# Optimization experiments

Measured on AMD Instinct MI355X. Metric: run time of the kernel, lower is better.

Reference implementation:

```python
import jax, jax.numpy as jnp
import numpy as np

N_ACTOR = 128
NUM_MODS = 6
NUM_PTS = 30
N = 32768
B = 64
EPS = 1e-5


def _gn(x, g, b):
    # torch GroupNorm(1, C) on [..., C]: normalize over channel axis, affine
    m = jnp.mean(x, axis=-1, keepdims=True)
    v = jnp.mean((x - m) ** 2, axis=-1, keepdims=True)
    return (x - m) * jax.lax.rsqrt(v + EPS) * g + b


def setup_inputs() -> dict:
    key = jax.random.key(0)
    ks = jax.random.split(key, 32)
    d = N_ACTOR
    M = NUM_MODS
    s = 0.05
    rn = lambda k, shp: jax.random.normal(k, shp, jnp.float32) * s
    inp = {
        'actors': jax.random.normal(ks[0], (N, d), jnp.float32),
        'actor_ctrs': jax.random.normal(ks[1], (N, 2), jnp.float32),
        'actor_idcs': jnp.arange(N, dtype=jnp.int32).reshape(B, N // B),
        # per-mode residual MLP + output linear (stacked over modes)
        'pred_W1': rn(ks[2], (M, d, d)),
        'pred_g1': jnp.ones((M, d), jnp.float32),
        'pred_b1': jnp.zeros((M, d), jnp.float32),
        'pred_W2': rn(ks[3], (M, d, d)),
        'pred_g2': jnp.ones((M, d), jnp.float32),
        'pred_b2': jnp.zeros((M, d), jnp.float32),
        'pred_Wo': rn(ks[4], (M, d, 2 * NUM_PTS)),
        'pred_bo': rn(ks[5], (M, 2 * NUM_PTS)),
        # cls head: residual MLP + Linear(d,1)
        'cls_W1': rn(ks[6], (d, d)),
        'cls_g1': jnp.ones((d,), jnp.float32),
        'cls_b1': jnp.zeros((d,), jnp.float32),
        'cls_W2': rn(ks[7], (d, d)),
        'cls_g2': jnp.ones((d,), jnp.float32),
        'cls_b2': jnp.zeros((d,), jnp.float32),
        'cls_Wo': rn(ks[8], (d, 1)),
        'cls_bo': rn(ks[9], (1,)),
        # AttDest
        'att_dW1': rn(ks[10], (2, d)),
        'att_db1': rn(ks[11], (d,)),
        'att_dW2': rn(ks[12], (d, d)),
        'att_dg2': jnp.ones((d,), jnp.float32),
        'att_db2': jnp.zeros((d,), jnp.float32),
        'att_aW': rn(ks[13], (2 * d, d)),
        'att_ag': jnp.ones((d,), jnp.float32),
        'att_ab': jnp.zeros((d,), jnp.float32),
    }
    return inp


def reference(actors, actor_ctrs, actor_idcs, pred_W1, pred_g1, pred_b1,
              pred_W2, pred_g2, pred_b2, pred_Wo, pred_bo,
              cls_W1, cls_g1, cls_b1, cls_W2, cls_g2, cls_b2, cls_Wo, cls_bo,
              att_dW1, att_db1, att_dW2, att_dg2, att_db2,
              att_aW, att_ag, att_ab):
    n = actors.shape[0]
    M = pred_W1.shape[0]
    h = jnp.einsum('nc,mcd->mnd', actors, pred_W1)              # [M,N,d]
    h = jax.nn.relu(_gn(h, pred_g1[:, None, :], pred_b1[:, None, :]))
    h = _gn(jnp.einsum('mnd,mde->mne', h, pred_W2),
            pred_g2[:, None, :], pred_b2[:, None, :])
    h = jax.nn.relu(h + actors[None])                           # residual
    preds = jnp.einsum('mnd,mdo->mno', h, pred_Wo) + pred_bo[:, None, :]
    reg = preds.transpose(1, 0, 2).reshape(n, M, NUM_PTS, 2)    # [N,M,T,2]
    # per-scene reg[idcs] += ctrs: actor_idcs partitions arange(N), so this
    # is exactly a per-actor broadcast add of the (concatenated) centers
    reg = reg + actor_ctrs[:, None, None, :]
    dest_ctrs = jax.lax.stop_gradient(reg[:, :, -1, :])         # .detach()
    # --- AttDest ---
    dist = (actor_ctrs[:, None, :] - dest_ctrs).reshape(-1, 2)  # [N*M,2]
    dist = jax.nn.relu(dist @ att_dW1 + att_db1)
    dist = jax.nn.relu(_gn(dist @ att_dW2, att_dg2, att_db2))
    agts = jnp.broadcast_to(actors[:, None, :], (n, M, actors.shape[1]))
    agts = agts.reshape(-1, actors.shape[1])
    feats = jax.nn.relu(_gn(jnp.concatenate([dist, agts], axis=1) @ att_aW,
                            att_ag, att_ab))                    # [N*M,d]
    # --- cls head ---
    c = jax.nn.relu(_gn(feats @ cls_W1, cls_g1, cls_b1))
    c = _gn(c @ cls_W2, cls_g2, cls_b2)
    c = jax.nn.relu(c + feats)
    cls = (c @ cls_Wo + cls_bo).reshape(n, M)
    # --- sort modes by descending score, reorder reg accordingly ---
    order = jnp.argsort(-cls, axis=1)
    cls = jnp.take_along_axis(cls, order, axis=1)
    reg = jnp.take_along_axis(reg, order[:, :, None, None], axis=1)
    # train_model=True concatenates the per-scene splits back in order,
    # which reproduces the full arrays
    return cls, reg
```

## Files before the change

kernel.cpp:

```cpp
#include <hip/hip_runtime.h>

#define EPSV 1e-5f
#define CLS_SZ (32768*6)
#define FWS_FLOATS ((size_t)196608 * 128)

#define AL(ch,row) (((ch)<<7) + ((row) ^ ((((ch)&15))<<3)))

__device__ __forceinline__ float4 ld4(const float* p) { return *reinterpret_cast<const float4*>(p); }
__device__ __forceinline__ void st4(float* p, float4 v) { *reinterpret_cast<float4*>(p) = v; }

__device__ __forceinline__ void ldW2(const float* __restrict__ Wg, int k0, int jg4,
                                     float4 (&w0)[2], float4 (&w1)[2])
{
  #pragma unroll
  for (int kk = 0; kk < 2; ++kk) {
    w0[kk] = ld4(Wg + (k0 + kk)*128 + jg4);
    w1[kk] = ld4(Wg + (k0 + kk)*128 + 64 + jg4);
  }
}

__device__ __forceinline__ void fma2(const float* X, int k0, int ag,
                                     const float4 (&w0)[2], const float4 (&w1)[2],
                                     float (&acc)[8][8])
{
  #pragma unroll
  for (int kk = 0; kk < 2; ++kk) {
    int k = k0 + kk;
    const float* xp = X + (k<<7) + ((ag<<3) ^ ((k & 15)<<3));
    float4 x0 = ld4(xp), x1 = ld4(xp + 4);
    float xv[8] = {x0.x,x0.y,x0.z,x0.w,x1.x,x1.y,x1.z,x1.w};
    float wv[8] = {w0[kk].x,w0[kk].y,w0[kk].z,w0[kk].w,
                   w1[kk].x,w1[kk].y,w1[kk].z,w1[kk].w};
    #pragma unroll
    for (int r = 0; r < 8; ++r)
      #pragma unroll
      for (int c2 = 0; c2 < 8; ++c2)
        acc[r][c2] = fmaf(xv[r], wv[c2], acc[r][c2]);
  }
}

__device__ __forceinline__ void gemmR(const float* X, const float* __restrict__ Wg,
                                      float (&acc)[8][8], int ag, int jg4)
{
  float4 a0[2], a1[2], b0[2], b1[2];
  ldW2(Wg, 0, jg4, a0, a1);
  #pragma unroll 1
  for (int c = 0; c < 64; c += 2) {
    ldW2(Wg, (c+1)*2, jg4, b0, b1);
    fma2(X, c*2, ag, a0, a1, acc);
    if (c + 2 < 64) ldW2(Wg, (c+2)*2, jg4, a0, a1);
    fma2(X, (c+1)*2, ag, b0, b1, acc);
  }
}

__device__ __forceinline__ void ldWo(const float* __restrict__ Wg, int k0, int jg,
                                     bool ldw, float4 (&w)[8])
{
  #pragma unroll
  for (int kk = 0; kk < 8; ++kk)
    w[kk] = ldw ? ld4(Wg + (k0 + kk)*60 + jg*4) : make_float4(0.f,0.f,0.f,0.f);
}

__device__ __forceinline__ void fmaWo(const float* X, int k0, int ag,
                                      const float4 (&w)[8], float (&acc)[8][4])
{
  #pragma unroll
  for (int kk = 0; kk < 8; ++kk) {
    int k = k0 + kk;
    const float* xp = X + (k<<7) + ((ag<<3) ^ ((k & 15)<<3));
    float4 x0 = ld4(xp), x1 = ld4(xp + 4);
    float xv[8] = {x0.x,x0.y,x0.z,x0.w,x1.x,x1.y,x1.z,x1.w};
    float wv[4] = {w[kk].x,w[kk].y,w[kk].z,w[kk].w};
    #pragma unroll
    for (int r = 0; r < 8; ++r)
      #pragma unroll
      for (int c2 = 0; c2 < 4; ++c2)
        acc[r][c2] = fmaf(xv[r], wv[c2], acc[r][c2]);
  }
}

__device__ __forceinline__ void gemmWoR(const float* X, const float* __restrict__ Wg,
                                        float (&acc)[8][4], int ag, int jg)
{
  const bool ldw = (jg < 15);
  float4 a[8], b[8];
  ldWo(Wg, 0, jg, ldw, a);
  #pragma unroll 1
  for (int c = 0; c < 16; c += 2) {
    ldWo(Wg, (c+1)*8, jg, ldw, b);
    fmaWo(X, c*8, ag, a, acc);
    if (c + 2 < 16) ldWo(Wg, (c+2)*8, jg, ldw, a);
    fmaWo(X, (c+1)*8, ag, b, acc);
  }
}

__device__ __forceinline__ void gn_finish(float* PS1, float* PS2, float* MEAN, float* RSTD, int tid)
{
  __syncthreads();
  if (tid < 128) {
    float a = 0.f, b = 0.f;
    #pragma unroll
    for (int j = 0; j < 4; ++j) { a += PS1[tid*4 + j]; b += PS2[tid*4 + j]; }
    float mu = a * 0.0078125f;
    float var = b * 0.0078125f - mu*mu;
    MEAN[tid] = mu;
    RSTD[tid] = rsqrtf(var + EPSV);
  }
  __syncthreads();
}

__device__ __forceinline__ void gn_reduce8(const float (&acc)[8][8], float* PS1, float* PS2,
                                           float* MEAN, float* RSTD, int ag, int jg, int tid)
{
  #pragma unroll
  for (int r = 0; r < 8; ++r) {
    float s = 0.f, q = 0.f;
    #pragma unroll
    for (int c = 0; c < 8; ++c) { float v = acc[r][c]; s += v; q += v*v; }
    s += __shfl_xor(s, 1, 64); q += __shfl_xor(q, 1, 64);
    s += __shfl_xor(s, 2, 64); q += __shfl_xor(q, 2, 64);
    if ((jg & 3) == 0) { int row = ag*8 + r; PS1[row*4 + (jg>>2)] = s; PS2[row*4 + (jg>>2)] = q; }
  }
  gn_finish(PS1, PS2, MEAN, RSTD, tid);
}

__global__ void __launch_bounds__(256, 2) pred_kernel(
    const float* __restrict__ actors, const float* __restrict__ ctrs,
    const float* __restrict__ W1, const float* __restrict__ g1v, const float* __restrict__ b1v,
    const float* __restrict__ W2, const float* __restrict__ g2v, const float* __restrict__ b2v,
    const float* __restrict__ Wo, const float* __restrict__ bov,
    float* __restrict__ out_reg)
{
  __shared__ __align__(16) float ACT[16384];
  __shared__ float PS1[512], PS2[512], MEAN[128], RSTD[128];

  const int tid = threadIdx.x;
  const int jg = tid & 15, ag = tid >> 4;
  const int jg4 = jg*4;
  const int m  = blockIdx.y;
  const int n0 = blockIdx.x * 128;

  #pragma unroll
  for (int p = 0; p < 16; ++p) {
    int i = (p<<8) + tid;
    int r = i >> 5, q4 = (i & 31) << 2;
    float4 v = ld4(actors + (size_t)(n0 + r)*128 + q4);
    ACT[AL(q4+0, r)] = v.x; ACT[AL(q4+1, r)] = v.y;
    ACT[AL(q4+2, r)] = v.z; ACT[AL(q4+3, r)] = v.w;
  }
  __syncthreads();

  float acc[8][8];
  #pragma unroll
  for (int r = 0; r < 8; ++r)
    #pragma unroll
    for (int c = 0; c < 8; ++c) acc[r][c] = 0.f;

  gemmR(ACT, W1 + (size_t)m*16384, acc, ag, jg4);
  gn_reduce8(acc, PS1, PS2, MEAN, RSTD, ag, jg, tid);
  {
    float mu[8], rs[8];
    #pragma unroll
    for (int r = 0; r < 8; ++r) { mu[r] = MEAN[ag*8+r]; rs[r] = RSTD[ag*8+r]; }
    float4 gl = ld4(g1v + m*128 + jg4), gh = ld4(g1v + m*128 + 64 + jg4);
    float4 bl = ld4(b1v + m*128 + jg4), bh = ld4(b1v + m*128 + 64 + jg4);
    float gv[8] = {gl.x,gl.y,gl.z,gl.w,gh.x,gh.y,gh.z,gh.w};
    float bv[8] = {bl.x,bl.y,bl.z,bl.w,bh.x,bh.y,bh.z,bh.w};
    float vm[8][8];
    #pragma unroll
    for (int r = 0; r < 8; ++r)
      #pragma unroll
      for (int c = 0; c < 8; ++c)
        vm[r][c] = fmaxf((acc[r][c] - mu[r]) * rs[r] * gv[c] + bv[c], 0.f);
    #pragma unroll
    for (int c = 0; c < 8; ++c) {
      int ch = (c < 4) ? (jg4 + c) : (64 + jg4 + (c - 4));
      int base = (ch<<7) + ((ag<<3) ^ ((ch & 15)<<3));
      st4(ACT + base,     make_float4(vm[0][c],vm[1][c],vm[2][c],vm[3][c]));
      st4(ACT + base + 4, make_float4(vm[4][c],vm[5][c],vm[6][c],vm[7][c]));
    }
  }
  __syncthreads();

  #pragma unroll
  for (int r = 0; r < 8; ++r)
    #pragma unroll
    for (int c = 0; c < 8; ++c) acc[r][c] = 0.f;

  gemmR(ACT, W2 + (size_t)m*16384, acc, ag, jg4);
  gn_reduce8(acc, PS1, PS2, MEAN, RSTD, ag, jg, tid);
  {
    float mu[8], rs[8];
    #pragma unroll
    for (int r = 0; r < 8; ++r) { mu[r] = MEAN[ag*8+r]; rs[r] = RSTD[ag*8+r]; }
    float4 gl = ld4(g2v + m*128 + jg4), gh = ld4(g2v + m*128 + 64 + jg4);
    float4 bl = ld4(b2v + m*128 + jg4), bh = ld4(b2v + m*128 + 64 + jg4);
    float gv[8] = {gl.x,gl.y,gl.z,gl.w,gh.x,gh.y,gh.z,gh.w};
    float bv[8] = {bl.x,bl.y,bl.z,bl.w,bh.x,bh.y,bh.z,bh.w};
    float vm[8][8];
    #pragma unroll
    for (int r = 0; r < 8; ++r) {
      const float* ap = actors + (size_t)(n0 + ag*8 + r)*128;
      float4 a0 = ld4(ap + jg4), a1 = ld4(ap + 64 + jg4);
      float av[8] = {a0.x,a0.y,a0.z,a0.w,a1.x,a1.y,a1.z,a1.w};
      #pragma unroll
      for (int c = 0; c < 8; ++c)
        vm[r][c] = fmaxf((acc[r][c] - mu[r]) * rs[r] * gv[c] + bv[c] + av[c], 0.f);
    }
    #pragma unroll
    for (int c = 0; c < 8; ++c) {
      int ch = (c < 4) ? (jg4 + c) : (64 + jg4 + (c - 4));
      int base = (ch<<7) + ((ag<<3) ^ ((ch & 15)<<3));
      st4(ACT + base,     make_float4(vm[0][c],vm[1][c],vm[2][c],vm[3][c]));
      st4(ACT + base + 4, make_float4(vm[4][c],vm[5][c],vm[6][c],vm[7][c]));
    }
  }
  __syncthreads();

  float acc2[8][4];
  #pragma unroll
  for (int r = 0; r < 8; ++r)
    #pragma unroll
    for (int c = 0; c < 4; ++c) acc2[r][c] = 0.f;
  gemmWoR(ACT, Wo + (size_t)m*7680, acc2, ag, jg);

  if (jg < 15) {
    float4 bo4 = ld4(bov + m*60 + jg4);
    #pragma unroll
    for (int r = 0; r < 8; ++r) {
      int n = n0 + ag*8 + r;
      float2 cc = *reinterpret_cast<const float2*>(ctrs + 2*n);
      float4 v;
      v.x = acc2[r][0] + bo4.x + cc.x;
      v.y = acc2[r][1] + bo4.y + cc.y;
      v.z = acc2[r][2] + bo4.z + cc.x;
      v.w = acc2[r][3] + bo4.w + cc.y;
      st4(out_reg + (size_t)n*360 + m*60 + jg4, v);
    }
  }
}

__global__ void __launch_bounds__(256, 2) att_feats_kernel(
    const float* __restrict__ actors, const float* __restrict__ ctrs,
    const float* __restrict__ dW1, const float* __restrict__ db1,
    const float* __restrict__ dW2, const float* __restrict__ dg2, const float* __restrict__ db2,
    const float* __restrict__ aW, const float* __restrict__ aG, const float* __restrict__ aB,
    const float* __restrict__ reg, float* __restrict__ fws)
{
  __shared__ __align__(16) float ACT[16384];
  __shared__ float PS1[512], PS2[512], MEAN[128], RSTD[128];
  float* D0x = MEAN;
  float* D0y = RSTD;

  const int tid = threadIdx.x;
  const int jg = tid & 15, ag = tid >> 4;
  const int jg4 = jg*4;
  const int r0 = blockIdx.x * 128;

  if (tid < 128) {
    int rg = r0 + tid;
    int n = rg / 6, mm = rg - 6*n;
    size_t base = (size_t)n*360 + mm*60;
    float2 c2 = *reinterpret_cast<const float2*>(ctrs + 2*n);
    D0x[tid] = c2.x - reg[base + 58];
    D0y[tid] = c2.y - reg[base + 59];
  }
  __syncthreads();

  {
    float dx[8], dy[8];
    #pragma unroll
    for (int r = 0; r < 8; ++r) { dx[r] = D0x[ag*8+r]; dy[r] = D0y[ag*8+r]; }
    #pragma unroll
    for (int c = 0; c < 8; ++c) {
      int ch = (c < 4) ? (jg4 + c) : (64 + jg4 + (c - 4));
      float w1 = dW1[ch], w2 = dW1[128 + ch], bb = db1[ch];
      float v[8];
      #pragma unroll
      for (int r = 0; r < 8; ++r) v[r] = fmaxf(fmaf(dx[r], w1, fmaf(dy[r], w2, bb)), 0.f);
      int base = (ch<<7) + ((ag<<3) ^ ((ch & 15)<<3));
      st4(ACT + base,     make_float4(v[0],v[1],v[2],v[3]));
      st4(ACT + base + 4, make_float4(v[4],v[5],v[6],v[7]));
    }
  }
  __syncthreads();

  float acc[8][8];
  #pragma unroll
  for (int r = 0; r < 8; ++r)
    #pragma unroll
    for (int c = 0; c < 8; ++c) acc[r][c] = 0.f;

  gemmR(ACT, dW2, acc, ag, jg4);
  gn_reduce8(acc, PS1, PS2, MEAN, RSTD, ag, jg, tid);
  {
    float mu[8], rs[8];
    #pragma unroll
    for (int r = 0; r < 8; ++r) { mu[r] = MEAN[ag*8+r]; rs[r] = RSTD[ag*8+r]; }
    float4 gl = ld4(dg2 + jg4), gh = ld4(dg2 + 64 + jg4);
    float4 bl = ld4(db2 + jg4), bh = ld4(db2 + 64 + jg4);
    float gv[8] = {gl.x,gl.y,gl.z,gl.w,gh.x,gh.y,gh.z,gh.w};
    float bv[8] = {bl.x,bl.y,bl.z,bl.w,bh.x,bh.y,bh.z,bh.w};
    float vm[8][8];
    #pragma unroll
    for (int r = 0; r < 8; ++r)
      #pragma unroll
      for (int c = 0; c < 8; ++c)
        vm[r][c] = fmaxf((acc[r][c] - mu[r]) * rs[r] * gv[c] + bv[c], 0.f);
    #pragma unroll
    for (int c = 0; c < 8; ++c) {
      int ch = (c < 4) ? (jg4 + c) : (64 + jg4 + (c - 4));
      int base = (ch<<7) + ((ag<<3) ^ ((ch & 15)<<3));
      st4(ACT + base,     make_float4(vm[0][c],vm[1][c],vm[2][c],vm[3][c]));
      st4(ACT + base + 4, make_float4(vm[4][c],vm[5][c],vm[6][c],vm[7][c]));
    }
  }
  __syncthreads();

  #pragma unroll
  for (int r = 0; r < 8; ++r)
    #pragma unroll
    for (int c = 0; c < 8; ++c) acc[r][c] = 0.f;
  gemmR(ACT, aW, acc, ag, jg4);
  __syncthreads();
  #pragma unroll
  for (int p = 0; p < 16; ++p) {
    int i = (p<<8) + tid;
    int r = i >> 5, q4 = (i & 31) << 2;
    int n = (r0 + r) / 6;
    float4 v = ld4(actors + (size_t)n*128 + q4);
    ACT[AL(q4+0, r)] = v.x; ACT[AL(q4+1, r)] = v.y;
    ACT[AL(q4+2, r)] = v.z; ACT[AL(q4+3, r)] = v.w;
  }
  __syncthreads();
  gemmR(ACT, aW + 16384, acc, ag, jg4);
  gn_reduce8(acc, PS1, PS2, MEAN, RSTD, ag, jg, tid);
  {
    float mu[8], rs[8];
    #pragma unroll
    for (int r = 0; r < 8; ++r) { mu[r] = MEAN[ag*8+r]; rs[r] = RSTD[ag*8+r]; }
    float4 gl = ld4(aG + jg4), gh = ld4(aG + 64 + jg4);
    float4 bl = ld4(aB + jg4), bh = ld4(aB + 64 + jg4);
    float gv[8] = {gl.x,gl.y,gl.z,gl.w,gh.x,gh.y,gh.z,gh.w};
    float bv[8] = {bl.x,bl.y,bl.z,bl.w,bh.x,bh.y,bh.z,bh.w};
    #pragma unroll
    for (int r = 0; r < 8; ++r) {
      float fv[8];
      #pragma unroll
      for (int c = 0; c < 8; ++c)
        fv[c] = fmaxf((acc[r][c] - mu[r]) * rs[r] * gv[c] + bv[c], 0.f);
      float* fp = fws + (size_t)(r0 + ag*8 + r)*128;
      st4(fp + jg4,      make_float4(fv[0],fv[1],fv[2],fv[3]));
      st4(fp + 64 + jg4, make_float4(fv[4],fv[5],fv[6],fv[7]));
    }
  }
}

__global__ void __launch_bounds__(256, 2) att_cls2_kernel(
    const float* __restrict__ cW1, const float* __restrict__ cg1, const float* __restrict__ cb1,
    const float* __restrict__ cW2, const float* __restrict__ cg2, const float* __restrict__ cb2,
    const float* __restrict__ cWo, const float* __restrict__ cbo,
    const float* __restrict__ fws, float* __restrict__ cls_out)
{
  __shared__ __align__(16) float ACT[16384];
  __shared__ float PS1[512], PS2[512], MEAN[128], RSTD[128];

  const int tid = threadIdx.x;
  const int jg = tid & 15, ag = tid >> 4;
  const int jg4 = jg*4;
  const int r0 = blockIdx.x * 128;

  #pragma unroll
  for (int p = 0; p < 16; ++p) {
    int i = (p<<8) + tid;
    int r = i >> 5, q4 = (i & 31) << 2;
    float4 v = ld4(fws + (size_t)(r0 + r)*128 + q4);
    ACT[AL(q4+0, r)] = v.x; ACT[AL(q4+1, r)] = v.y;
    ACT[AL(q4+2, r)] = v.z; ACT[AL(q4+3, r)] = v.w;
  }
  __syncthreads();

  float acc[8][8];
  #pragma unroll
  for (int r = 0; r < 8; ++r)
    #pragma unroll
    for (int c = 0; c < 8; ++c) acc[r][c] = 0.f;

  gemmR(ACT, cW1, acc, ag, jg4);
  gn_reduce8(acc, PS1, PS2, MEAN, RSTD, ag, jg, tid);
  {
    float mu[8], rs[8];
    #pragma unroll
    for (int r = 0; r < 8; ++r) { mu[r] = MEAN[ag*8+r]; rs[r] = RSTD[ag*8+r]; }
    float4 gl = ld4(cg1 + jg4), gh = ld4(cg1 + 64 + jg4);
    float4 bl = ld4(cb1 + jg4), bh = ld4(cb1 + 64 + jg4);
    float gv[8] = {gl.x,gl.y,gl.z,gl.w,gh.x,gh.y,gh.z,gh.w};
    float bv[8] = {bl.x,bl.y,bl.z,bl.w,bh.x,bh.y,bh.z,bh.w};
    float vm[8][8];
    #pragma unroll
    for (int r = 0; r < 8; ++r)
      #pragma unroll
      for (int c = 0; c < 8; ++c)
        vm[r][c] = fmaxf((acc[r][c] - mu[r]) * rs[r] * gv[c] + bv[c], 0.f);
    #pragma unroll
    for (int c = 0; c < 8; ++c) {
      int ch = (c < 4) ? (jg4 + c) : (64 + jg4 + (c - 4));
      int base = (ch<<7) + ((ag<<3) ^ ((ch & 15)<<3));
      st4(ACT + base,     make_float4(vm[0][c],vm[1][c],vm[2][c],vm[3][c]));
      st4(ACT + base + 4, make_float4(vm[4][c],vm[5][c],vm[6][c],vm[7][c]));
    }
  }
  __syncthreads();

  #pragma unroll
  for (int r = 0; r < 8; ++r)
    #pragma unroll
    for (int c = 0; c < 8; ++c) acc[r][c] = 0.f;
  gemmR(ACT, cW2, acc, ag, jg4);
  gn_reduce8(acc, PS1, PS2, MEAN, RSTD, ag, jg, tid);
  {
    float mu[8], rs[8];
    #pragma unroll
    for (int r = 0; r < 8; ++r) { mu[r] = MEAN[ag*8+r]; rs[r] = RSTD[ag*8+r]; }
    float4 gl = ld4(cg2 + jg4), gh = ld4(cg2 + 64 + jg4);
    float4 bl = ld4(cb2 + jg4), bh = ld4(cb2 + 64 + jg4);
    float4 wl = ld4(cWo + jg4), wh = ld4(cWo + 64 + jg4);
    float gv[8] = {gl.x,gl.y,gl.z,gl.w,gh.x,gh.y,gh.z,gh.w};
    float bv[8] = {bl.x,bl.y,bl.z,bl.w,bh.x,bh.y,bh.z,bh.w};
    float wv[8] = {wl.x,wl.y,wl.z,wl.w,wh.x,wh.y,wh.z,wh.w};
    #pragma unroll
    for (int r = 0; r < 8; ++r) {
      const float* fp = fws + (size_t)(r0 + ag*8 + r)*128;
      float4 a0 = ld4(fp + jg4), a1 = ld4(fp + 64 + jg4);
      float av[8] = {a0.x,a0.y,a0.z,a0.w,a1.x,a1.y,a1.z,a1.w};
      float p = 0.f;
      #pragma unroll
      for (int c = 0; c < 8; ++c) {
        float v = (acc[r][c] - mu[r]) * rs[r] * gv[c] + bv[c];
        v = fmaxf(v + av[c], 0.f);
        p = fmaf(v, wv[c], p);
      }
      float s = p;
      s += __shfl_xor(s, 1, 64);
      s += __shfl_xor(s, 2, 64);
      if ((jg & 3) == 0) PS1[(ag*8+r)*4 + (jg>>2)] = s;
    }
  }
  __syncthreads();
  if (tid < 128) {
    float s = 0.f;
    #pragma unroll
    for (int j = 0; j < 4; ++j) s += PS1[tid*4 + j];
    cls_out[r0 + tid] = s + cbo[0];
  }
}

__global__ void __launch_bounds__(256, 2) att_cls_mono_kernel(
    const float* __restrict__ actors, const float* __restrict__ ctrs,
    const float* __restrict__ dW1, const float* __restrict__ db1,
    const float* __restrict__ dW2, const float* __restrict__ dg2, const float* __restrict__ db2,
    const float* __restrict__ aW, const float* __restrict__ aG, const float* __restrict__ aB,
    const float* __restrict__ cW1, const float* __restrict__ cg1, const float* __restrict__ cb1,
    const float* __restrict__ cW2, const float* __restrict__ cg2, const float* __restrict__ cb2,
    const float* __restrict__ cWo, const float* __restrict__ cbo,
    const float* __restrict__ reg, float* __restrict__ cls_out)
{
  __shared__ __align__(16) float ACT[16384];
  __shared__ float PS1[512], PS2[512], MEAN[128], RSTD[128];
  float* D0x = MEAN;
  float* D0y = RSTD;

  const int tid = threadIdx.x;
  const int jg = tid & 15, ag = tid >> 4;
  const int jg4 = jg*4;
  const int r0 = blockIdx.x * 128;

  if (tid < 128) {
    int rg = r0 + tid;
    int n = rg / 6, mm = rg - 6*n;
    size_t base = (size_t)n*360 + mm*60;
    float2 c2 = *reinterpret_cast<const float2*>(ctrs + 2*n);
    D0x[tid] = c2.x - reg[base + 58];
    D0y[tid] = c2.y - reg[base + 59];
  }
  __syncthreads();

  {
    float dx[8], dy[8];
    #pragma unroll
    for (int r = 0; r < 8; ++r) { dx[r] = D0x[ag*8+r]; dy[r] = D0y[ag*8+r]; }
    #pragma unroll
    for (int c = 0; c < 8; ++c) {
      int ch = (c < 4) ? (jg4 + c) : (64 + jg4 + (c - 4));
      float w1 = dW1[ch], w2 = dW1[128 + ch], bb = db1[ch];
      float v[8];
      #pragma unroll
      for (int r = 0; r < 8; ++r) v[r] = fmaxf(fmaf(dx[r], w1, fmaf(dy[r], w2, bb)), 0.f);
      int base = (ch<<7) + ((ag<<3) ^ ((ch & 15)<<3));
      st4(ACT + base,     make_float4(v[0],v[1],v[2],v[3]));
      st4(ACT + base + 4, make_float4(v[4],v[5],v[6],v[7]));
    }
  }
  __syncthreads();

  float acc[8][8];
  #pragma unroll
  for (int r = 0; r < 8; ++r)
    #pragma unroll
    for (int c = 0; c < 8; ++c) acc[r][c] = 0.f;

  gemmR(ACT, dW2, acc, ag, jg4);
  gn_reduce8(acc, PS1, PS2, MEAN, RSTD, ag, jg, tid);
  {
    float mu[8], rs[8];
    #pragma unroll
    for (int r = 0; r < 8; ++r) { mu[r] = MEAN[ag*8+r]; rs[r] = RSTD[ag*8+r]; }
    float4 gl = ld4(dg2 + jg4), gh = ld4(dg2 + 64 + jg4);
    float4 bl = ld4(db2 + jg4), bh = ld4(db2 + 64 + jg4);
    float gv[8] = {gl.x,gl.y,gl.z,gl.w,gh.x,gh.y,gh.z,gh.w};
    float bv[8] = {bl.x,bl.y,bl.z,bl.w,bh.x,bh.y,bh.z,bh.w};
    float vm[8][8];
    #pragma unroll
    for (int r = 0; r < 8; ++r)
      #pragma unroll
      for (int c = 0; c < 8; ++c)
        vm[r][c] = fmaxf((acc[r][c] - mu[r]) * rs[r] * gv[c] + bv[c], 0.f);
    #pragma unroll
    for (int c = 0; c < 8; ++c) {
      int ch = (c < 4) ? (jg4 + c) : (64 + jg4 + (c - 4));
      int base = (ch<<7) + ((ag<<3) ^ ((ch & 15)<<3));
      st4(ACT + base,     make_float4(vm[0][c],vm[1][c],vm[2][c],vm[3][c]));
      st4(ACT + base + 4, make_float4(vm[4][c],vm[5][c],vm[6][c],vm[7][c]));
    }
  }
  __syncthreads();

  #pragma unroll
  for (int r = 0; r < 8; ++r)
    #pragma unroll
    for (int c = 0; c < 8; ++c) acc[r][c] = 0.f;
  gemmR(ACT, aW, acc, ag, jg4);
  __syncthreads();
  #pragma unroll
  for (int p = 0; p < 16; ++p) {
    int i = (p<<8) + tid;
    int r = i >> 5, q4 = (i & 31) << 2;
    int n = (r0 + r) / 6;
    float4 v = ld4(actors + (size_t)n*128 + q4);
    ACT[AL(q4+0, r)] = v.x; ACT[AL(q4+1, r)] = v.y;
    ACT[AL(q4+2, r)] = v.z; ACT[AL(q4+3, r)] = v.w;
  }
  __syncthreads();
  gemmR(ACT, aW + 16384, acc, ag, jg4);
  gn_reduce8(acc, PS1, PS2, MEAN, RSTD, ag, jg, tid);
  float feats[8][8];
  {
    float mu[8], rs[8];
    #pragma unroll
    for (int r = 0; r < 8; ++r) { mu[r] = MEAN[ag*8+r]; rs[r] = RSTD[ag*8+r]; }
    float4 gl = ld4(aG + jg4), gh = ld4(aG + 64 + jg4);
    float4 bl = ld4(aB + jg4), bh = ld4(aB + 64 + jg4);
    float gv[8] = {gl.x,gl.y,gl.z,gl.w,gh.x,gh.y,gh.z,gh.w};
    float bv[8] = {bl.x,bl.y,bl.z,bl.w,bh.x,bh.y,bh.z,bh.w};
    #pragma unroll
    for (int r = 0; r < 8; ++r)
      #pragma unroll
      for (int c = 0; c < 8; ++c)
        feats[r][c] = fmaxf((acc[r][c] - mu[r]) * rs[r] * gv[c] + bv[c], 0.f);
    #pragma unroll
    for (int c = 0; c < 8; ++c) {
      int ch = (c < 4) ? (jg4 + c) : (64 + jg4 + (c - 4));
      int base = (ch<<7) + ((ag<<3) ^ ((ch & 15)<<3));
      st4(ACT + base,     make_float4(feats[0][c],feats[1][c],feats[2][c],feats[3][c]));
      st4(ACT + base + 4, make_float4(feats[4][c],feats[5][c],feats[6][c],feats[7][c]));
    }
  }
  __syncthreads();

  #pragma unroll
  for (int r = 0; r < 8; ++r)
    #pragma unroll
    for (int c = 0; c < 8; ++c) acc[r][c] = 0.f;
  gemmR(ACT, cW1, acc, ag, jg4);
  gn_reduce8(acc, PS1, PS2, MEAN, RSTD, ag, jg, tid);
  {
    float mu[8], rs[8];
    #pragma unroll
    for (int r = 0; r < 8; ++r) { mu[r] = MEAN[ag*8+r]; rs[r] = RSTD[ag*8+r]; }
    float4 gl = ld4(cg1 + jg4), gh = ld4(cg1 + 64 + jg4);
    float4 bl = ld4(cb1 + jg4), bh = ld4(cb1 + 64 + jg4);
    float gv[8] = {gl.x,gl.y,gl.z,gl.w,gh.x,gh.y,gh.z,gh.w};
    float bv[8] = {bl.x,bl.y,bl.z,bl.w,bh.x,bh.y,bh.z,bh.w};
    float vm[8][8];
    #pragma unroll
    for (int r = 0; r < 8; ++r)
      #pragma unroll
      for (int c = 0; c < 8; ++c)
        vm[r][c] = fmaxf((acc[r][c] - mu[r]) * rs[r] * gv[c] + bv[c], 0.f);
    #pragma unroll
    for (int c = 0; c < 8; ++c) {
      int ch = (c < 4) ? (jg4 + c) : (64 + jg4 + (c - 4));
      int base = (ch<<7) + ((ag<<3) ^ ((ch & 15)<<3));
      st4(ACT + base,     make_float4(vm[0][c],vm[1][c],vm[2][c],vm[3][c]));
      st4(ACT + base + 4, make_float4(vm[4][c],vm[5][c],vm[6][c],vm[7][c]));
    }
  }
  __syncthreads();

  #pragma unroll
  for (int r = 0; r < 8; ++r)
    #pragma unroll
    for (int c = 0; c < 8; ++c) acc[r][c] = 0.f;
  gemmR(ACT, cW2, acc, ag, jg4);
  gn_reduce8(acc, PS1, PS2, MEAN, RSTD, ag, jg, tid);
  {
    float mu[8], rs[8], p[8];
    #pragma unroll
    for (int r = 0; r < 8; ++r) { mu[r] = MEAN[ag*8+r]; rs[r] = RSTD[ag*8+r]; p[r] = 0.f; }
    float4 gl = ld4(cg2 + jg4), gh = ld4(cg2 + 64 + jg4);
    float4 bl = ld4(cb2 + jg4), bh = ld4(cb2 + 64 + jg4);
    float4 wl = ld4(cWo + jg4), wh = ld4(cWo + 64 + jg4);
    float gv[8] = {gl.x,gl.y,gl.z,gl.w,gh.x,gh.y,gh.z,gh.w};
    float bv[8] = {bl.x,bl.y,bl.z,bl.w,bh.x,bh.y,bh.z,bh.w};
    float wv[8] = {wl.x,wl.y,wl.z,wl.w,wh.x,wh.y,wh.z,wh.w};
    #pragma unroll
    for (int c = 0; c < 8; ++c) {
      #pragma unroll
      for (int r = 0; r < 8; ++r) {
        float v = (acc[r][c] - mu[r]) * rs[r] * gv[c] + bv[c];
        v = fmaxf(v + feats[r][c], 0.f);
        p[r] = fmaf(v, wv[c], p[r]);
      }
    }
    #pragma unroll
    for (int r = 0; r < 8; ++r) {
      float s = p[r];
      s += __shfl_xor(s, 1, 64);
      s += __shfl_xor(s, 2, 64);
      if ((jg & 3) == 0) PS1[(ag*8+r)*4 + (jg>>2)] = s;
    }
  }
  __syncthreads();
  if (tid < 128) {
    float s = 0.f;
    #pragma unroll
    for (int j = 0; j < 4; ++j) s += PS1[tid*4 + j];
    cls_out[r0 + tid] = s + cbo[0];
  }
}

__global__ void __launch_bounds__(256) sort_kernel(float* __restrict__ out)
{
  __shared__ float RL[64*360];
  __shared__ float CL[64*6];
  __shared__ float CS[64*6];
  __shared__ int   ORD[64*6];

  const int tid = threadIdx.x;
  const int n0 = blockIdx.x * 64;
  float* regp = out + CLS_SZ;

  for (int i = tid; i < 64*360; i += 256) RL[i] = regp[(size_t)n0*360 + i];
  for (int i = tid; i < 384; i += 256)    CL[i] = out[n0*6 + i];
  __syncthreads();

  if (tid < 64) {
    float v[6];
    #pragma unroll
    for (int m2 = 0; m2 < 6; ++m2) v[m2] = CL[tid*6 + m2];
    int used = 0;
    for (int j = 0; j < 6; ++j) {
      int best = -1; float bv = 0.f;
      for (int m2 = 0; m2 < 6; ++m2) {
        if (used & (1 << m2)) continue;
        if (best < 0 || v[m2] > bv) { best = m2; bv = v[m2]; }
      }
      used |= (1 << best);
      ORD[tid*6 + j] = best;
      CS[tid*6 + j] = bv;
    }
  }
  __syncthreads();

  for (int i = tid; i < 384; i += 256) out[n0*6 + i] = CS[i];
  for (int i = tid; i < 64*360; i += 256) {
    int rl = i / 360, rem = i - rl*360;
    int slot = rem / 60, j = rem - slot*60;
    out[CLS_SZ + (size_t)n0*360 + i] = RL[rl*360 + ORD[rl*6 + slot]*60 + j];
  }
}

extern "C" void kernel_launch(void* const* d_in, const int* in_sizes, int n_in,
                              void* d_out, int out_size, void* d_ws, size_t ws_size,
                              hipStream_t stream)
{
  (void)in_sizes; (void)n_in; (void)out_size;
  const float* actors = (const float*)d_in[0];
  const float* ctrs   = (const float*)d_in[1];
  const float* pW1 = (const float*)d_in[3];
  const float* pg1 = (const float*)d_in[4];
  const float* pb1 = (const float*)d_in[5];
  const float* pW2 = (const float*)d_in[6];
  const float* pg2 = (const float*)d_in[7];
  const float* pb2 = (const float*)d_in[8];
  const float* pWo = (const float*)d_in[9];
  const float* pbo = (const float*)d_in[10];
  const float* cW1 = (const float*)d_in[11];
  const float* cg1 = (const float*)d_in[12];
  const float* cb1 = (const float*)d_in[13];
  const float* cW2 = (const float*)d_in[14];
  const float* cg2 = (const float*)d_in[15];
  const float* cb2 = (const float*)d_in[16];
  const float* cWo = (const float*)d_in[17];
  const float* cbo = (const float*)d_in[18];
  const float* dW1 = (const float*)d_in[19];
  const float* db1 = (const float*)d_in[20];
  const float* dW2 = (const float*)d_in[21];
  const float* dg2 = (const float*)d_in[22];
  const float* db2 = (const float*)d_in[23];
  const float* aW  = (const float*)d_in[24];
  const float* aG  = (const float*)d_in[25];
  const float* aB  = (const float*)d_in[26];

  float* out = (float*)d_out;
  float* out_reg = out + CLS_SZ;
  float* fws = (float*)d_ws;
  const bool split = ws_size >= FWS_FLOATS * sizeof(float);

  dim3 gA(256, 6);
  pred_kernel<<<gA, 256, 0, stream>>>(actors, ctrs, pW1, pg1, pb1, pW2, pg2, pb2,
                                      pWo, pbo, out_reg);
  if (split) {
    att_feats_kernel<<<1536, 256, 0, stream>>>(actors, ctrs,
                                               dW1, db1, dW2, dg2, db2,
                                               aW, aG, aB, out_reg, fws);
    att_cls2_kernel<<<1536, 256, 0, stream>>>(cW1, cg1, cb1, cW2, cg2, cb2,
                                              cWo, cbo, fws, out);
  } else {
    att_cls_mono_kernel<<<1536, 256, 0, stream>>>(actors, ctrs,
                                                  dW1, db1, dW2, dg2, db2,
                                                  aW, aG, aB,
                                                  cW1, cg1, cb1, cW2, cg2, cb2, cWo, cbo,
                                                  out_reg, out);
  }
  sort_kernel<<<512, 256, 0, stream>>>(out);
}
```

Measured before the change: 789.9 us.

## Shrink row tile to 64 rows per block to raise occupancy

New measurement: 934.6 us. 18.3% more time.

```diff
diff --git a/kernel.cpp b/kernel.cpp
--- a/kernel.cpp
+++ b/kernel.cpp
@@ -5,6 +5,7 @@
 #define FWS_FLOATS ((size_t)196608 * 128)
 
 #define AL(ch,row) (((ch)<<7) + ((row) ^ ((((ch)&15))<<3)))
+#define AL64(ch,row) (((ch)<<6) + ((row) ^ ((((ch)&7))<<3)))
 
 __device__ __forceinline__ float4 ld4(const float* p) { return *reinterpret_cast<const float4*>(p); }
 __device__ __forceinline__ void st4(float* p, float4 v) { *reinterpret_cast<float4*>(p) = v; }
@@ -16,6 +17,432 @@
   for (int kk = 0; kk < 2; ++kk) {
     w0[kk] = ld4(Wg + (k0 + kk)*128 + jg4);
     w1[kk] = ld4(Wg + (k0 + kk)*128 + 64 + jg4);
+  }
+}
+
+__device__ __forceinline__ void fma2_64(const float* X, int k0, int ag,
+                                        const float4 (&w0)[2], const float4 (&w1)[2],
+                                        float (&acc)[4][8])
+{
+  #pragma unroll
+  for (int kk = 0; kk < 2; ++kk) {
+    int k = k0 + kk;
+    float4 x = ld4(X + (k<<6) + ((ag<<2) ^ ((k & 7)<<3)));
+    float xv[4] = {x.x,x.y,x.z,x.w};
+    float wv[8] = {w0[kk].x,w0[kk].y,w0[kk].z,w0[kk].w,
+                   w1[kk].x,w1[kk].y,w1[kk].z,w1[kk].w};
+    #pragma unroll
+    for (int r = 0; r < 4; ++r)
+      #pragma unroll
+      for (int c2 = 0; c2 < 8; ++c2)
+        acc[r][c2] = fmaf(xv[r], wv[c2], acc[r][c2]);
+  }
+}
+
+__device__ __forceinline__ void gemmR64(const float* X, const float* __restrict__ Wg,
+                                        float (&acc)[4][8], int ag, int jg4)
+{
+  float4 a0[2], a1[2], b0[2], b1[2];
+  ldW2(Wg, 0, jg4, a0, a1);
+  #pragma unroll 1
+  for (int c = 0; c < 64; c += 2) {
+    ldW2(Wg, (c+1)*2, jg4, b0, b1);
+    fma2_64(X, c*2, ag, a0, a1, acc);
+    if (c + 2 < 64) ldW2(Wg, (c+2)*2, jg4, a0, a1);
+    fma2_64(X, (c+1)*2, ag, b0, b1, acc);
+  }
+}
+
+__device__ __forceinline__ void ldWo(const float* __restrict__ Wg, int k0, int jg,
+                                     bool ldw, float4 (&w)[8])
+{
+  #pragma unroll
+  for (int kk = 0; kk < 8; ++kk)
+    w[kk] = ldw ? ld4(Wg + (k0 + kk)*60 + jg*4) : make_float4(0.f,0.f,0.f,0.f);
+}
+
+__device__ __forceinline__ void fmaWo64(const float* X, int k0, int ag,
+                                        const float4 (&w)[8], float (&acc)[4][4])
+{
+  #pragma unroll
+  for (int kk = 0; kk < 8; ++kk) {
+    int k = k0 + kk;
+    float4 x = ld4(X + (k<<6) + ((ag<<2) ^ ((k & 7)<<3)));
+    float xv[4] = {x.x,x.y,x.z,x.w};
+    float wv[4] = {w[kk].x,w[kk].y,w[kk].z,w[kk].w};
+    #pragma unroll
+    for (int r = 0; r < 4; ++r)
+      #pragma unroll
+      for (int c2 = 0; c2 < 4; ++c2)
+        acc[r][c2] = fmaf(xv[r], wv[c2], acc[r][c2]);
+  }
+}
+
+__device__ __forceinline__ void gemmWoR64(const float* X, const float* __restrict__ Wg,
+                                          float (&acc)[4][4], int ag, int jg)
+{
+  const bool ldw = (jg < 15);
+  float4 a[8], b[8];
+  ldWo(Wg, 0, jg, ldw, a);
+  #pragma unroll 1
+  for (int c = 0; c < 16; c += 2) {
+    ldWo(Wg, (c+1)*8, jg, ldw, b);
+    fmaWo64(X, c*8, ag, a, acc);
+    if (c + 2 < 16) ldWo(Wg, (c+2)*8, jg, ldw, a);
+    fmaWo64(X, (c+1)*8, ag, b, acc);
+  }
+}
+
+__device__ __forceinline__ void gn_finish64(float* PS1, float* PS2, float* MEAN, float* RSTD, int tid)
+{
+  __syncthreads();
+  if (tid < 64) {
+    float a = 0.f, b = 0.f;
+    #pragma unroll
+    for (int j = 0; j < 4; ++j) { a += PS1[tid*4 + j]; b += PS2[tid*4 + j]; }
+    float mu = a * 0.0078125f;
+    float var = b * 0.0078125f - mu*mu;
+    MEAN[tid] = mu;
+    RSTD[tid] = rsqrtf(var + EPSV);
+  }
+  __syncthreads();
+}
+
+__device__ __forceinline__ void gn_reduce4_64(const float (&acc)[4][8], float* PS1, float* PS2,
+                                              float* MEAN, float* RSTD, int ag, int jg, int tid)
+{
+  #pragma unroll
+  for (int r = 0; r < 4; ++r) {
+    float s = 0.f, q = 0.f;
+    #pragma unroll
+    for (int c = 0; c < 8; ++c) { float v = acc[r][c]; s += v; q += v*v; }
+    s += __shfl_xor(s, 1, 64); q += __shfl_xor(q, 1, 64);
+    s += __shfl_xor(s, 2, 64); q += __shfl_xor(q, 2, 64);
+    if ((jg & 3) == 0) { int row = ag*4 + r; PS1[row*4 + (jg>>2)] = s; PS2[row*4 + (jg>>2)] = q; }
+  }
+  gn_finish64(PS1, PS2, MEAN, RSTD, tid);
+}
+
+__global__ void __launch_bounds__(256, 4) pred_kernel(
+    const float* __restrict__ actors, const float* __restrict__ ctrs,
+    const float* __restrict__ W1, const float* __restrict__ g1v, const float* __restrict__ b1v,
+    const float* __restrict__ W2, const float* __restrict__ g2v, const float* __restrict__ b2v,
+    const float* __restrict__ Wo, const float* __restrict__ bov,
+    float* __restrict__ out_reg)
+{
+  __shared__ __align__(16) float ACT[8192];
+  __shared__ float PS1[256], PS2[256], MEAN[64], RSTD[64];
+
+  const int tid = threadIdx.x;
+  const int jg = tid & 15, ag = tid >> 4;
+  const int jg4 = jg*4;
+  const int m  = blockIdx.y;
+  const int n0 = blockIdx.x * 64;
+
+  #pragma unroll
+  for (int p = 0; p < 8; ++p) {
+    int i = (p<<8) + tid;
+    int r = i & 63, ch0 = (i >> 6) << 2;
+    float4 v = ld4(actors + (size_t)(n0 + r)*128 + ch0);
+    ACT[AL64(ch0+0, r)] = v.x; ACT[AL64(ch0+1, r)] = v.y;
+    ACT[AL64(ch0+2, r)] = v.z; ACT[AL64(ch0+3, r)] = v.w;
+  }
+  __syncthreads();
+
+  float acc[4][8];
+  #pragma unroll
+  for (int r = 0; r < 4; ++r)
+    #pragma unroll
+    for (int c = 0; c < 8; ++c) acc[r][c] = 0.f;
+
+  gemmR64(ACT, W1 + (size_t)m*16384, acc, ag, jg4);
+  gn_reduce4_64(acc, PS1, PS2, MEAN, RSTD, ag, jg, tid);
+  {
+    float mu[4], rs[4];
+    #pragma unroll
+    for (int r = 0; r < 4; ++r) { mu[r] = MEAN[ag*4+r]; rs[r] = RSTD[ag*4+r]; }
+    float4 gl = ld4(g1v + m*128 + jg4), gh = ld4(g1v + m*128 + 64 + jg4);
+    float4 bl = ld4(b1v + m*128 + jg4), bh = ld4(b1v + m*128 + 64 + jg4);
+    float gv[8] = {gl.x,gl.y,gl.z,gl.w,gh.x,gh.y,gh.z,gh.w};
+    float bv[8] = {bl.x,bl.y,bl.z,bl.w,bh.x,bh.y,bh.z,bh.w};
+    float vm[4][8];
+    #pragma unroll
+    for (int r = 0; r < 4; ++r)
+      #pragma unroll
+      for (int c = 0; c < 8; ++c)
+        vm[r][c] = fmaxf((acc[r][c] - mu[r]) * rs[r] * gv[c] + bv[c], 0.f);
+    #pragma unroll
+    for (int c = 0; c < 8; ++c) {
+      int ch = (c < 4) ? (jg4 + c) : (64 + jg4 + (c - 4));
+      st4(ACT + AL64(ch, ag*4), make_float4(vm[0][c],vm[1][c],vm[2][c],vm[3][c]));
+    }
+  }
+  __syncthreads();
+
+  #pragma unroll
+  for (int r = 0; r < 4; ++r)
+    #pragma unroll
+    for (int c = 0; c < 8; ++c) acc[r][c] = 0.f;
+
+  gemmR64(ACT, W2 + (size_t)m*16384, acc, ag, jg4);
+  gn_reduce4_64(acc, PS1, PS2, MEAN, RSTD, ag, jg, tid);
+  {
+    float mu[4], rs[4];
+    #pragma unroll
+    for (int r = 0; r < 4; ++r) { mu[r] = MEAN[ag*4+r]; rs[r] = RSTD[ag*4+r]; }
+    float4 gl = ld4(g2v + m*128 + jg4), gh = ld4(g2v + m*128 + 64 + jg4);
+    float4 bl = ld4(b2v + m*128 + jg4), bh = ld4(b2v + m*128 + 64 + jg4);
+    float gv[8] = {gl.x,gl.y,gl.z,gl.w,gh.x,gh.y,gh.z,gh.w};
+    float bv[8] = {bl.x,bl.y,bl.z,bl.w,bh.x,bh.y,bh.z,bh.w};
+    float vm[4][8];
+    #pragma unroll
+    for (int r = 0; r < 4; ++r) {
+      const float* ap = actors + (size_t)(n0 + ag*4 + r)*128;
+      float4 a0 = ld4(ap + jg4), a1 = ld4(ap + 64 + jg4);
+      float av[8] = {a0.x,a0.y,a0.z,a0.w,a1.x,a1.y,a1.z,a1.w};
+      #pragma unroll
+      for (int c = 0; c < 8; ++c)
+        vm[r][c] = fmaxf((acc[r][c] - mu[r]) * rs[r] * gv[c] + bv[c] + av[c], 0.f);
+    }
+    #pragma unroll
+    for (int c = 0; c < 8; ++c) {
+      int ch = (c < 4) ? (jg4 + c) : (64 + jg4 + (c - 4));
+      st4(ACT + AL64(ch, ag*4), make_float4(vm[0][c],vm[1][c],vm[2][c],vm[3][c]));
+    }
+  }
+  __syncthreads();
+
+  float acc2[4][4];
+  #pragma unroll
+  for (int r = 0; r < 4; ++r)
+    #pragma unroll
+    for (int c = 0; c < 4; ++c) acc2[r][c] = 0.f;
+  gemmWoR64(ACT, Wo + (size_t)m*7680, acc2, ag, jg);
+
+  if (jg < 15) {
+    float4 bo4 = ld4(bov + m*60 + jg4);
+    #pragma unroll
+    for (int r = 0; r < 4; ++r) {
+      int n = n0 + ag*4 + r;
+      float2 cc = *reinterpret_cast<const float2*>(ctrs + 2*n);
+      float4 v;
+      v.x = acc2[r][0] + bo4.x + cc.x;
+      v.y = acc2[r][1] + bo4.y + cc.y;
+      v.z = acc2[r][2] + bo4.z + cc.x;
+      v.w = acc2[r][3] + bo4.w + cc.y;
+      st4(out_reg + (size_t)n*360 + m*60 + jg4, v);
+    }
+  }
+}
+
+__global__ void __launch_bounds__(256, 4) att_feats_kernel(
+    const float* __restrict__ actors, const float* __restrict__ ctrs,
+    const float* __restrict__ dW1, const float* __restrict__ db1,
+    const float* __restrict__ dW2, const float* __restrict__ dg2, const float* __restrict__ db2,
+    const float* __restrict__ aW, const float* __restrict__ aG, const float* __restrict__ aB,
+    const float* __restrict__ reg, float* __restrict__ fws)
+{
+  __shared__ __align__(16) float ACT[8192];
+  __shared__ float PS1[256], PS2[256], MEAN[64], RSTD[64];
+  float* D0x = MEAN;
+  float* D0y = RSTD;
+
+  const int tid = threadIdx.x;
+  const int jg = tid & 15, ag = tid >> 4;
+  const int jg4 = jg*4;
+  const int r0 = blockIdx.x * 64;
+
+  if (tid < 64) {
+    int rg = r0 + tid;
+    int n = rg / 6, mm = rg - 6*n;
+    size_t base = (size_t)n*360 + mm*60;
+    float2 c2 = *reinterpret_cast<const float2*>(ctrs + 2*n);
+    D0x[tid] = c2.x - reg[base + 58];
+    D0y[tid] = c2.y - reg[base + 59];
+  }
+  __syncthreads();
+
+  {
+    float dx[4], dy[4];
+    #pragma unroll
+    for (int r = 0; r < 4; ++r) { dx[r] = D0x[ag*4+r]; dy[r] = D0y[ag*4+r]; }
+    #pragma unroll
+    for (int c = 0; c < 8; ++c) {
+      int ch = (c < 4) ? (jg4 + c) : (64 + jg4 + (c - 4));
+      float w1 = dW1[ch], w2 = dW1[128 + ch], bb = db1[ch];
+      float4 v;
+      v.x = fmaxf(fmaf(dx[0], w1, fmaf(dy[0], w2, bb)), 0.f);
+      v.y = fmaxf(fmaf(dx[1], w1, fmaf(dy[1], w2, bb)), 0.f);
+      v.z = fmaxf(fmaf(dx[2], w1, fmaf(dy[2], w2, bb)), 0.f);
+      v.w = fmaxf(fmaf(dx[3], w1, fmaf(dy[3], w2, bb)), 0.f);
+      st4(ACT + AL64(ch, ag*4), v);
+    }
+  }
+  __syncthreads();
+
+  float acc[4][8];
+  #pragma unroll
+  for (int r = 0; r < 4; ++r)
+    #pragma unroll
+    for (int c = 0; c < 8; ++c) acc[r][c] = 0.f;
+
+  gemmR64(ACT, dW2, acc, ag, jg4);
+  gn_reduce4_64(acc, PS1, PS2, MEAN, RSTD, ag, jg, tid);
+  {
+    float mu[4], rs[4];
+    #pragma unroll
+    for (int r = 0; r < 4; ++r) { mu[r] = MEAN[ag*4+r]; rs[r] = RSTD[ag*4+r]; }
+    float4 gl = ld4(dg2 + jg4), gh = ld4(dg2 + 64 + jg4);
+    float4 bl = ld4(db2 + jg4), bh = ld4(db2 + 64 + jg4);
+    float gv[8] = {gl.x,gl.y,gl.z,gl.w,gh.x,gh.y,gh.z,gh.w};
+    float bv[8] = {bl.x,bl.y,bl.z,bl.w,bh.x,bh.y,bh.z,bh.w};
+    float vm[4][8];
+    #pragma unroll
+    for (int r = 0; r < 4; ++r)
+      #pragma unroll
+      for (int c = 0; c < 8; ++c)
+        vm[r][c] = fmaxf((acc[r][c] - mu[r]) * rs[r] * gv[c] + bv[c], 0.f);
+    #pragma unroll
+    for (int c = 0; c < 8; ++c) {
+      int ch = (c < 4) ? (jg4 + c) : (64 + jg4 + (c - 4));
+      st4(ACT + AL64(ch, ag*4), make_float4(vm[0][c],vm[1][c],vm[2][c],vm[3][c]));
+    }
+  }
+  __syncthreads();
+
+  #pragma unroll
+  for (int r = 0; r < 4; ++r)
+    #pragma unroll
+    for (int c = 0; c < 8; ++c) acc[r][c] = 0.f;
+  gemmR64(ACT, aW, acc, ag, jg4);
+  __syncthreads();
+  #pragma unroll
+  for (int p = 0; p < 8; ++p) {
+    int i = (p<<8) + tid;
+    int r = i & 63, ch0 = (i >> 6) << 2;
+    int n = (r0 + r) / 6;
+    float4 v = ld4(actors + (size_t)n*128 + ch0);
+    ACT[AL64(ch0+0, r)] = v.x; ACT[AL64(ch0+1, r)] = v.y;
+    ACT[AL64(ch0+2, r)] = v.z; ACT[AL64(ch0+3, r)] = v.w;
+  }
+  __syncthreads();
+  gemmR64(ACT, aW + 16384, acc, ag, jg4);
+  gn_reduce4_64(acc, PS1, PS2, MEAN, RSTD, ag, jg, tid);
+  {
+    float mu[4], rs[4];
+    #pragma unroll
+    for (int r = 0; r < 4; ++r) { mu[r] = MEAN[ag*4+r]; rs[r] = RSTD[ag*4+r]; }
+    float4 gl = ld4(aG + jg4), gh = ld4(aG + 64 + jg4);
+    float4 bl = ld4(aB + jg4), bh = ld4(aB + 64 + jg4);
+    float gv[8] = {gl.x,gl.y,gl.z,gl.w,gh.x,gh.y,gh.z,gh.w};
+    float bv[8] = {bl.x,bl.y,bl.z,bl.w,bh.x,bh.y,bh.z,bh.w};
+    #pragma unroll
+    for (int r = 0; r < 4; ++r) {
+      float fv[8];
+      #pragma unroll
+      for (int c = 0; c < 8; ++c)
+        fv[c] = fmaxf((acc[r][c] - mu[r]) * rs[r] * gv[c] + bv[c], 0.f);
+      float* fp = fws + (size_t)(r0 + ag*4 + r)*128;
+      st4(fp + jg4,      make_float4(fv[0],fv[1],fv[2],fv[3]));
+      st4(fp + 64 + jg4, make_float4(fv[4],fv[5],fv[6],fv[7]));
+    }
+  }
+}
+
+__global__ void __launch_bounds__(256, 4) att_cls2_kernel(
+    const float* __restrict__ cW1, const float* __restrict__ cg1, const float* __restrict__ cb1,
+    const float* __restrict__ cW2, const float* __restrict__ cg2, const float* __restrict__ cb2,
+    const float* __restrict__ cWo, const float* __restrict__ cbo,
+    const float* __restrict__ fws, float* __restrict__ cls_out)
+{
+  __shared__ __align__(16) float ACT[8192];
+  __shared__ float PS1[256], PS2[256], MEAN[64], RSTD[64];
+
+  const int tid = threadIdx.x;
+  const int jg = tid & 15, ag = tid >> 4;
+  const int jg4 = jg*4;
+  const int r0 = blockIdx.x * 64;
+
+  #pragma unroll
+  for (int p = 0; p < 8; ++p) {
+    int i = (p<<8) + tid;
+    int r = i & 63, ch0 = (i >> 6) << 2;
+    float4 v = ld4(fws + (size_t)(r0 + r)*128 + ch0);
+    ACT[AL64(ch0+0, r)] = v.x; ACT[AL64(ch0+1, r)] = v.y;
+    ACT[AL64(ch0+2, r)] = v.z; ACT[AL64(ch0+3, r)] = v.w;
+  }
+  __syncthreads();
+
+  float acc[4][8];
+  #pragma unroll
+  for (int r = 0; r < 4; ++r)
+    #pragma unroll
+    for (int c = 0; c < 8; ++c) acc[r][c] = 0.f;
+
+  gemmR64(ACT, cW1, acc, ag, jg4);
+  gn_reduce4_64(acc, PS1, PS2, MEAN, RSTD, ag, jg, tid);
+  {
+    float mu[4], rs[4];
+    #pragma unroll
+    for (int r = 0; r < 4; ++r) { mu[r] = MEAN[ag*4+r]; rs[r] = RSTD[ag*4+r]; }
+    float4 gl = ld4(cg1 + jg4), gh = ld4(cg1 + 64 + jg4);
+    float4 bl = ld4(cb1 + jg4), bh = ld4(cb1 + 64 + jg4);
+    float gv[8] = {gl.x,gl.y,gl.z,gl.w,gh.x,gh.y,gh.z,gh.w};
+    float bv[8] = {bl.x,bl.y,bl.z,bl.w,bh.x,bh.y,bh.z,bh.w};
+    float vm[4][8];
+    #pragma unroll
+    for (int r = 0; r < 4; ++r)
+      #pragma unroll
+      for (int c = 0; c < 8; ++c)
+        vm[r][c] = fmaxf((acc[r][c] - mu[r]) * rs[r] * gv[c] + bv[c], 0.f);
+    #pragma unroll
+    for (int c = 0; c < 8; ++c) {
+      int ch = (c < 4) ? (jg4 + c) : (64 + jg4 + (c - 4));
+      st4(ACT + AL64(ch, ag*4), make_float4(vm[0][c],vm[1][c],vm[2][c],vm[3][c]));
+    }
+  }
+  __syncthreads();
+
+  #pragma unroll
+  for (int r = 0; r < 4; ++r)
+    #pragma unroll
+    for (int c = 0; c < 8; ++c) acc[r][c] = 0.f;
+  gemmR64(ACT, cW2, acc, ag, jg4);
+  gn_reduce4_64(acc, PS1, PS2, MEAN, RSTD, ag, jg, tid);
+  {
+    float mu[4], rs[4];
+    #pragma unroll
+    for (int r = 0; r < 4; ++r) { mu[r] = MEAN[ag*4+r]; rs[r] = RSTD[ag*4+r]; }
+    float4 gl = ld4(cg2 + jg4), gh = ld4(cg2 + 64 + jg4);
+    float4 bl = ld4(cb2 + jg4), bh = ld4(cb2 + 64 + jg4);
+    float4 wl = ld4(cWo + jg4), wh = ld4(cWo + 64 + jg4);
+    float gv[8] = {gl.x,gl.y,gl.z,gl.w,gh.x,gh.y,gh.z,gh.w};
+    float bv[8] = {bl.x,bl.y,bl.z,bl.w,bh.x,bh.y,bh.z,bh.w};
+    float wv[8] = {wl.x,wl.y,wl.z,wl.w,wh.x,wh.y,wh.z,wh.w};
+    #pragma unroll
+    for (int r = 0; r < 4; ++r) {
+      const float* fp = fws + (size_t)(r0 + ag*4 + r)*128;
+      float4 a0 = ld4(fp + jg4), a1 = ld4(fp + 64 + jg4);
+      float av[8] = {a0.x,a0.y,a0.z,a0.w,a1.x,a1.y,a1.z,a1.w};
+      float p = 0.f;
+      #pragma unroll
+      for (int c = 0; c < 8; ++c) {
+        float v = (acc[r][c] - mu[r]) * rs[r] * gv[c] + bv[c];
+        v = fmaxf(v + av[c], 0.f);
+        p = fmaf(v, wv[c], p);
+      }
+      float s = p;
+      s += __shfl_xor(s, 1, 64);
+      s += __shfl_xor(s, 2, 64);
+      if ((jg & 3) == 0) PS1[(ag*4+r)*4 + (jg>>2)] = s;
+    }
+  }
+  __syncthreads();
+  if (tid < 64) {
+    float s = 0.f;
+    #pragma unroll
+    for (int j = 0; j < 4; ++j) s += PS1[tid*4 + j];
+    cls_out[r0 + tid] = s + cbo[0];
   }
 }
 
@@ -53,48 +480,7 @@
   }
 }
 
-__device__ __forceinline__ void ldWo(const float* __restrict__ Wg, int k0, int jg,
-                                     bool ldw, float4 (&w)[8])
-{
-  #pragma unroll
-  for (int kk = 0; kk < 8; ++kk)
-    w[kk] = ldw ? ld4(Wg + (k0 + kk)*60 + jg*4) : make_float4(0.f,0.f,0.f,0.f);
-}
-
-__device__ __forceinline__ void fmaWo(const float* X, int k0, int ag,
-                                      const float4 (&w)[8], float (&acc)[8][4])
-{
-  #pragma unroll
-  for (int kk = 0; kk < 8; ++kk) {
-    int k = k0 + kk;
-    const float* xp = X + (k<<7) + ((ag<<3) ^ ((k & 15)<<3));
-    float4 x0 = ld4(xp), x1 = ld4(xp + 4);
-    float xv[8] = {x0.x,x0.y,x0.z,x0.w,x1.x,x1.y,x1.z,x1.w};
-    float wv[4] = {w[kk].x,w[kk].y,w[kk].z,w[kk].w};
-    #pragma unroll
-    for (int r = 0; r < 8; ++r)
-      #pragma unroll
-      for (int c2 = 0; c2 < 4; ++c2)
-        acc[r][c2] = fmaf(xv[r], wv[c2], acc[r][c2]);
-  }
-}
-
-__device__ __forceinline__ void gemmWoR(const float* X, const float* __restrict__ Wg,
-                                        float (&acc)[8][4], int ag, int jg)
-{
-  const bool ldw = (jg < 15);
-  float4 a[8], b[8];
-  ldWo(Wg, 0, jg, ldw, a);
-  #pragma unroll 1
-  for (int c = 0; c < 16; c += 2) {
-    ldWo(Wg, (c+1)*8, jg, ldw, b);
-    fmaWo(X, c*8, ag, a, acc);
-    if (c + 2 < 16) ldWo(Wg, (c+2)*8, jg, ldw, a);
-    fmaWo(X, (c+1)*8, ag, b, acc);
-  }
-}
-
-__device__ __forceinline__ void gn_finish(float* PS1, float* PS2, float* MEAN, float* RSTD, int tid)
+__device__ __forceinline__ void gn_finish128(float* PS1, float* PS2, float* MEAN, float* RSTD, int tid)
 {
   __syncthreads();
   if (tid < 128) {
@@ -121,338 +507,7 @@
     s += __shfl_xor(s, 2, 64); q += __shfl_xor(q, 2, 64);
     if ((jg & 3) == 0) { int row = ag*8 + r; PS1[row*4 + (jg>>2)] = s; PS2[row*4 + (jg>>2)] = q; }
   }
-  gn_finish(PS1, PS2, MEAN, RSTD, tid);
-}
-
-__global__ void __launch_bounds__(256, 2) pred_kernel(
-    const float* __restrict__ actors, const float* __restrict__ ctrs,
-    const float* __restrict__ W1, const float* __restrict__ g1v, const float* __restrict__ b1v,
-    const float* __restrict__ W2, const float* __restrict__ g2v, const float* __restrict__ b2v,
-    const float* __restrict__ Wo, const float* __restrict__ bov,
-    float* __restrict__ out_reg)
-{
-  __shared__ __align__(16) float ACT[16384];
-  __shared__ float PS1[512], PS2[512], MEAN[128], RSTD[128];
-
-  const int tid = threadIdx.x;
-  const int jg = tid & 15, ag = tid >> 4;
-  const int jg4 = jg*4;
-  const int m  = blockIdx.y;
-  const int n0 = blockIdx.x * 128;
-
-  #pragma unroll
-  for (int p = 0; p < 16; ++p) {
-    int i = (p<<8) + tid;
-    int r = i >> 5, q4 = (i & 31) << 2;
-    float4 v = ld4(actors + (size_t)(n0 + r)*128 + q4);
-    ACT[AL(q4+0, r)] = v.x; ACT[AL(q4+1, r)] = v.y;
-    ACT[AL(q4+2, r)] = v.z; ACT[AL(q4+3, r)] = v.w;
-  }
-  __syncthreads();
-
-  float acc[8][8];
-  #pragma unroll
-  for (int r = 0; r < 8; ++r)
-    #pragma unroll
-    for (int c = 0; c < 8; ++c) acc[r][c] = 0.f;
-
-  gemmR(ACT, W1 + (size_t)m*16384, acc, ag, jg4);
-  gn_reduce8(acc, PS1, PS2, MEAN, RSTD, ag, jg, tid);
-  {
-    float mu[8], rs[8];
-    #pragma unroll
-    for (int r = 0; r < 8; ++r) { mu[r] = MEAN[ag*8+r]; rs[r] = RSTD[ag*8+r]; }
-    float4 gl = ld4(g1v + m*128 + jg4), gh = ld4(g1v + m*128 + 64 + jg4);
-    float4 bl = ld4(b1v + m*128 + jg4), bh = ld4(b1v + m*128 + 64 + jg4);
-    float gv[8] = {gl.x,gl.y,gl.z,gl.w,gh.x,gh.y,gh.z,gh.w};
-    float bv[8] = {bl.x,bl.y,bl.z,bl.w,bh.x,bh.y,bh.z,bh.w};
-    float vm[8][8];
-    #pragma unroll
-    for (int r = 0; r < 8; ++r)
-      #pragma unroll
-      for (int c = 0; c < 8; ++c)
-        vm[r][c] = fmaxf((acc[r][c] - mu[r]) * rs[r] * gv[c] + bv[c], 0.f);
-    #pragma unroll
-    for (int c = 0; c < 8; ++c) {
-      int ch = (c < 4) ? (jg4 + c) : (64 + jg4 + (c - 4));
-      int base = (ch<<7) + ((ag<<3) ^ ((ch & 15)<<3));
-      st4(ACT + base,     make_float4(vm[0][c],vm[1][c],vm[2][c],vm[3][c]));
-      st4(ACT + base + 4, make_float4(vm[4][c],vm[5][c],vm[6][c],vm[7][c]));
-    }
-  }
-  __syncthreads();
-
-  #pragma unroll
-  for (int r = 0; r < 8; ++r)
-    #pragma unroll
-    for (int c = 0; c < 8; ++c) acc[r][c] = 0.f;
-
-  gemmR(ACT, W2 + (size_t)m*16384, acc, ag, jg4);
-  gn_reduce8(acc, PS1, PS2, MEAN, RSTD, ag, jg, tid);
-  {
-    float mu[8], rs[8];
-    #pragma unroll
-    for (int r = 0; r < 8; ++r) { mu[r] = MEAN[ag*8+r]; rs[r] = RSTD[ag*8+r]; }
-    float4 gl = ld4(g2v + m*128 + jg4), gh = ld4(g2v + m*128 + 64 + jg4);
-    float4 bl = ld4(b2v + m*128 + jg4), bh = ld4(b2v + m*128 + 64 + jg4);
-    float gv[8] = {gl.x,gl.y,gl.z,gl.w,gh.x,gh.y,gh.z,gh.w};
-    float bv[8] = {bl.x,bl.y,bl.z,bl.w,bh.x,bh.y,bh.z,bh.w};
-    float vm[8][8];
-    #pragma unroll
-    for (int r = 0; r < 8; ++r) {
-      const float* ap = actors + (size_t)(n0 + ag*8 + r)*128;
-      float4 a0 = ld4(ap + jg4), a1 = ld4(ap + 64 + jg4);
-      float av[8] = {a0.x,a0.y,a0.z,a0.w,a1.x,a1.y,a1.z,a1.w};
-      #pragma unroll
-      for (int c = 0; c < 8; ++c)
-        vm[r][c] = fmaxf((acc[r][c] - mu[r]) * rs[r] * gv[c] + bv[c] + av[c], 0.f);
-    }
-    #pragma unroll
-    for (int c = 0; c < 8; ++c) {
-      int ch = (c < 4) ? (jg4 + c) : (64 + jg4 + (c - 4));
-      int base = (ch<<7) + ((ag<<3) ^ ((ch & 15)<<3));
-      st4(ACT + base,     make_float4(vm[0][c],vm[1][c],vm[2][c],vm[3][c]));
-      st4(ACT + base + 4, make_float4(vm[4][c],vm[5][c],vm[6][c],vm[7][c]));
-    }
-  }
-  __syncthreads();
-
-  float acc2[8][4];
-  #pragma unroll
-  for (int r = 0; r < 8; ++r)
-    #pragma unroll
-    for (int c = 0; c < 4; ++c) acc2[r][c] = 0.f;
-  gemmWoR(ACT, Wo + (size_t)m*7680, acc2, ag, jg);
-
-  if (jg < 15) {
-    float4 bo4 = ld4(bov + m*60 + jg4);
-    #pragma unroll
-    for (int r = 0; r < 8; ++r) {
-      int n = n0 + ag*8 + r;
-      float2 cc = *reinterpret_cast<const float2*>(ctrs + 2*n);
-      float4 v;
-      v.x = acc2[r][0] + bo4.x + cc.x;
-      v.y = acc2[r][1] + bo4.y + cc.y;
-      v.z = acc2[r][2] + bo4.z + cc.x;
-      v.w = acc2[r][3] + bo4.w + cc.y;
-      st4(out_reg + (size_t)n*360 + m*60 + jg4, v);
-    }
-  }
-}
-
-__global__ void __launch_bounds__(256, 2) att_feats_kernel(
-    const float* __restrict__ actors, const float* __restrict__ ctrs,
-    const float* __restrict__ dW1, const float* __restrict__ db1,
-    const float* __restrict__ dW2, const float* __restrict__ dg2, const float* __restrict__ db2,
-    const float* __restrict__ aW, const float* __restrict__ aG, const float* __restrict__ aB,
-    const float* __restrict__ reg, float* __restrict__ fws)
-{
-  __shared__ __align__(16) float ACT[16384];
-  __shared__ float PS1[512], PS2[512], MEAN[128], RSTD[128];
-  float* D0x = MEAN;
-  float* D0y = RSTD;
-
-  const int tid = threadIdx.x;
-  const int jg = tid & 15, ag = tid >> 4;
-  const int jg4 = jg*4;
-  const int r0 = blockIdx.x * 128;
-
-  if (tid < 128) {
-    int rg = r0 + tid;
-    int n = rg / 6, mm = rg - 6*n;
-    size_t base = (size_t)n*360 + mm*60;
-    float2 c2 = *reinterpret_cast<const float2*>(ctrs + 2*n);
-    D0x[tid] = c2.x - reg[base + 58];
-    D0y[tid] = c2.y - reg[base + 59];
-  }
-  __syncthreads();
-
-  {
-    float dx[8], dy[8];
-    #pragma unroll
-    for (int r = 0; r < 8; ++r) { dx[r] = D0x[ag*8+r]; dy[r] = D0y[ag*8+r]; }
-    #pragma unroll
-    for (int c = 0; c < 8; ++c) {
-      int ch = (c < 4) ? (jg4 + c) : (64 + jg4 + (c - 4));
-      float w1 = dW1[ch], w2 = dW1[128 + ch], bb = db1[ch];
-      float v[8];
-      #pragma unroll
-      for (int r = 0; r < 8; ++r) v[r] = fmaxf(fmaf(dx[r], w1, fmaf(dy[r], w2, bb)), 0.f);
-      int base = (ch<<7) + ((ag<<3) ^ ((ch & 15)<<3));
-      st4(ACT + base,     make_float4(v[0],v[1],v[2],v[3]));
-      st4(ACT + base + 4, make_float4(v[4],v[5],v[6],v[7]));
-    }
-  }
-  __syncthreads();
-
-  float acc[8][8];
-  #pragma unroll
-  for (int r = 0; r < 8; ++r)
-    #pragma unroll
-    for (int c = 0; c < 8; ++c) acc[r][c] = 0.f;
-
-  gemmR(ACT, dW2, acc, ag, jg4);
-  gn_reduce8(acc, PS1, PS2, MEAN, RSTD, ag, jg, tid);
-  {
-    float mu[8], rs[8];
-    #pragma unroll
-    for (int r = 0; r < 8; ++r) { mu[r] = MEAN[ag*8+r]; rs[r] = RSTD[ag*8+r]; }
-    float4 gl = ld4(dg2 + jg4), gh = ld4(dg2 + 64 + jg4);
-    float4 bl = ld4(db2 + jg4), bh = ld4(db2 + 64 + jg4);
-    float gv[8] = {gl.x,gl.y,gl.z,gl.w,gh.x,gh.y,gh.z,gh.w};
-    float bv[8] = {bl.x,bl.y,bl.z,bl.w,bh.x,bh.y,bh.z,bh.w};
-    float vm[8][8];
-    #pragma unroll
-    for (int r = 0; r < 8; ++r)
-      #pragma unroll
-      for (int c = 0; c < 8; ++c)
-        vm[r][c] = fmaxf((acc[r][c] - mu[r]) * rs[r] * gv[c] + bv[c], 0.f);
-    #pragma unroll
-    for (int c = 0; c < 8; ++c) {
-      int ch = (c < 4) ? (jg4 + c) : (64 + jg4 + (c - 4));
-      int base = (ch<<7) + ((ag<<3) ^ ((ch & 15)<<3));
-      st4(ACT + base,     make_float4(vm[0][c],vm[1][c],vm[2][c],vm[3][c]));
-      st4(ACT + base + 4, make_float4(vm[4][c],vm[5][c],vm[6][c],vm[7][c]));
-    }
-  }
-  __syncthreads();
-
-  #pragma unroll
-  for (int r = 0; r < 8; ++r)
-    #pragma unroll
-    for (int c = 0; c < 8; ++c) acc[r][c] = 0.f;
-  gemmR(ACT, aW, acc, ag, jg4);
-  __syncthreads();
-  #pragma unroll
-  for (int p = 0; p < 16; ++p) {
-    int i = (p<<8) + tid;
-    int r = i >> 5, q4 = (i & 31) << 2;
-    int n = (r0 + r) / 6;
-    float4 v = ld4(actors + (size_t)n*128 + q4);
-    ACT[AL(q4+0, r)] = v.x; ACT[AL(q4+1, r)] = v.y;
-    ACT[AL(q4+2, r)] = v.z; ACT[AL(q4+3, r)] = v.w;
-  }
-  __syncthreads();
-  gemmR(ACT, aW + 16384, acc, ag, jg4);
-  gn_reduce8(acc, PS1, PS2, MEAN, RSTD, ag, jg, tid);
-  {
-    float mu[8], rs[8];
-    #pragma unroll
-    for (int r = 0; r < 8; ++r) { mu[r] = MEAN[ag*8+r]; rs[r] = RSTD[ag*8+r]; }
-    float4 gl = ld4(aG + jg4), gh = ld4(aG + 64 + jg4);
-    float4 bl = ld4(aB + jg4), bh = ld4(aB + 64 + jg4);
-    float gv[8] = {gl.x,gl.y,gl.z,gl.w,gh.x,gh.y,gh.z,gh.w};
-    float bv[8] = {bl.x,bl.y,bl.z,bl.w,bh.x,bh.y,bh.z,bh.w};
-    #pragma unroll
-    for (int r = 0; r < 8; ++r) {
-      float fv[8];
-      #pragma unroll
-      for (int c = 0; c < 8; ++c)
-        fv[c] = fmaxf((acc[r][c] - mu[r]) * rs[r] * gv[c] + bv[c], 0.f);
-      float* fp = fws + (size_t)(r0 + ag*8 + r)*128;
-      st4(fp + jg4,      make_float4(fv[0],fv[1],fv[2],fv[3]));
-      st4(fp + 64 + jg4, make_float4(fv[4],fv[5],fv[6],fv[7]));
-    }
-  }
-}
-
-__global__ void __launch_bounds__(256, 2) att_cls2_kernel(
-    const float* __restrict__ cW1, const float* __restrict__ cg1, const float* __restrict__ cb1,
-    const float* __restrict__ cW2, const float* __restrict__ cg2, const float* __restrict__ cb2,
-    const float* __restrict__ cWo, const float* __restrict__ cbo,
-    const float* __restrict__ fws, float* __restrict__ cls_out)
-{
-  __shared__ __align__(16) float ACT[16384];
-  __shared__ float PS1[512], PS2[512], MEAN[128], RSTD[128];
-
-  const int tid = threadIdx.x;
-  const int jg = tid & 15, ag = tid >> 4;
-  const int jg4 = jg*4;
-  const int r0 = blockIdx.x * 128;
-
-  #pragma unroll
-  for (int p = 0; p < 16; ++p) {
-    int i = (p<<8) + tid;
-    int r = i >> 5, q4 = (i & 31) << 2;
-    float4 v = ld4(fws + (size_t)(r0 + r)*128 + q4);
-    ACT[AL(q4+0, r)] = v.x; ACT[AL(q4+1, r)] = v.y;
-    ACT[AL(q4+2, r)] = v.z; ACT[AL(q4+3, r)] = v.w;
-  }
-  __syncthreads();
-
-  float acc[8][8];
-  #pragma unroll
-  for (int r = 0; r < 8; ++r)
-    #pragma unroll
-    for (int c = 0; c < 8; ++c) acc[r][c] = 0.f;
-
-  gemmR(ACT, cW1, acc, ag, jg4);
-  gn_reduce8(acc, PS1, PS2, MEAN, RSTD, ag, jg, tid);
-  {
-    float mu[8], rs[8];
-    #pragma unroll
-    for (int r = 0; r < 8; ++r) { mu[r] = MEAN[ag*8+r]; rs[r] = RSTD[ag*8+r]; }
-    float4 gl = ld4(cg1 + jg4), gh = ld4(cg1 + 64 + jg4);
-    float4 bl = ld4(cb1 + jg4), bh = ld4(cb1 + 64 + jg4);
-    float gv[8] = {gl.x,gl.y,gl.z,gl.w,gh.x,gh.y,gh.z,gh.w};
-    float bv[8] = {bl.x,bl.y,bl.z,bl.w,bh.x,bh.y,bh.z,bh.w};
-    float vm[8][8];
-    #pragma unroll
-    for (int r = 0; r < 8; ++r)
-      #pragma unroll
-      for (int c = 0; c < 8; ++c)
-        vm[r][c] = fmaxf((acc[r][c] - mu[r]) * rs[r] * gv[c] + bv[c], 0.f);
-    #pragma unroll
-    for (int c = 0; c < 8; ++c) {
-      int ch = (c < 4) ? (jg4 + c) : (64 + jg4 + (c - 4));
-      int base = (ch<<7) + ((ag<<3) ^ ((ch & 15)<<3));
-      st4(ACT + base,     make_float4(vm[0][c],vm[1][c],vm[2][c],vm[3][c]));
-      st4(ACT + base + 4, make_float4(vm[4][c],vm[5][c],vm[6][c],vm[7][c]));
-    }
-  }
-  __syncthreads();
-
-  #pragma unroll
-  for (int r = 0; r < 8; ++r)
-    #pragma unroll
-    for (int c = 0; c < 8; ++c) acc[r][c] = 0.f;
-  gemmR(ACT, cW2, acc, ag, jg4);
-  gn_reduce8(acc, PS1, PS2, MEAN, RSTD, ag, jg, tid);
-  {
-    float mu[8], rs[8];
-    #pragma unroll
-    for (int r = 0; r < 8; ++r) { mu[r] = MEAN[ag*8+r]; rs[r] = RSTD[ag*8+r]; }
-    float4 gl = ld4(cg2 + jg4), gh = ld4(cg2 + 64 + jg4);
-    float4 bl = ld4(cb2 + jg4), bh = ld4(cb2 + 64 + jg4);
-    float4 wl = ld4(cWo + jg4), wh = ld4(cWo + 64 + jg4);
-    float gv[8] = {gl.x,gl.y,gl.z,gl.w,gh.x,gh.y,gh.z,gh.w};
-    float bv[8] = {bl.x,bl.y,bl.z,bl.w,bh.x,bh.y,bh.z,bh.w};
-    float wv[8] = {wl.x,wl.y,wl.z,wl.w,wh.x,wh.y,wh.z,wh.w};
-    #pragma unroll
-    for (int r = 0; r < 8; ++r) {
-      const float* fp = fws + (size_t)(r0 + ag*8 + r)*128;
-      float4 a0 = ld4(fp + jg4), a1 = ld4(fp + 64 + jg4);
-      float av[8] = {a0.x,a0.y,a0.z,a0.w,a1.x,a1.y,a1.z,a1.w};
-      float p = 0.f;
-      #pragma unroll
-      for (int c = 0; c < 8; ++c) {
-        float v = (acc[r][c] - mu[r]) * rs[r] * gv[c] + bv[c];
-        v = fmaxf(v + av[c], 0.f);
-        p = fmaf(v, wv[c], p);
-      }
-      float s = p;
-      s += __shfl_xor(s, 1, 64);
-      s += __shfl_xor(s, 2, 64);
-      if ((jg & 3) == 0) PS1[(ag*8+r)*4 + (jg>>2)] = s;
-    }
-  }
-  __syncthreads();
-  if (tid < 128) {
-    float s = 0.f;
-    #pragma unroll
-    for (int j = 0; j < 4; ++j) s += PS1[tid*4 + j];
-    cls_out[r0 + tid] = s + cbo[0];
-  }
+  gn_finish128(PS1, PS2, MEAN, RSTD, tid);
 }
 
 __global__ void __launch_bounds__(256, 2) att_cls_mono_kernel(
@@ -727,14 +782,14 @@
   float* fws = (float*)d_ws;
   const bool split = ws_size >= FWS_FLOATS * sizeof(float);
 
-  dim3 gA(256, 6);
+  dim3 gA(512, 6);
   pred_kernel<<<gA, 256, 0, stream>>>(actors, ctrs, pW1, pg1, pb1, pW2, pg2, pb2,
                                       pWo, pbo, out_reg);
   if (split) {
-    att_feats_kernel<<<1536, 256, 0, stream>>>(actors, ctrs,
+    att_feats_kernel<<<3072, 256, 0, stream>>>(actors, ctrs,
                                                dW1, db1, dW2, dg2, db2,
                                                aW, aG, aB, out_reg, fws);
-    att_cls2_kernel<<<1536, 256, 0, stream>>>(cW1, cg1, cb1, cW2, cg2, cb2,
+    att_cls2_kernel<<<3072, 256, 0, stream>>>(cW1, cg1, cb1, cW2, cg2, cb2,
                                               cWo, cbo, fws, out);
   } else {
     att_cls_mono_kernel<<<1536, 256, 0, stream>>>(actors, ctrs,
```
